# Optimization experiments

Measured on AMD Instinct MI355X. Metric: run time of the kernel, lower is better.

Reference implementation:

```python
import jax, jax.numpy as jnp
import numpy as np

SINKHORN_ITERS = 20
EPS = 1e-6


def setup_inputs() -> dict:
    key = jax.random.key(0)
    k1, k2 = jax.random.split(key)
    x = jax.random.normal(k1, (4, 4096, 4096), dtype=jnp.float32)
    W = jax.random.normal(k2, (4096, 4096), dtype=jnp.float32) * 0.02
    return {"x": x, "W": W}


def _sinkhorn(W):
    # W: [N, N] logits -> doubly-stochastic (Birkhoff) matrix, unit marginals
    P = jnp.exp(W)

    def body(_, P):
        P = P * (1.0 / (P.sum(axis=-2, keepdims=True) + EPS))  # column normalize
        P = P * (1.0 / (P.sum(axis=-1, keepdims=True) + EPS))  # row normalize
        return P

    return jax.lax.fori_loop(0, SINKHORN_ITERS, body, P)


def reference(x, W):
    W_proj = _sinkhorn(W)          # [N, N]
    out = jnp.matmul(x, W_proj)    # [B, S, N] @ [N, N] -> [B, S, N]
    return out
```

## Files before the change

kernel.cpp:

```cpp
#include <hip/hip_runtime.h>
#include <hip/hip_bf16.h>
#include <cstdint>
#include <cstddef>

#define NN 4096
#define SINK_ITERS 20
#define EPSV 1e-6f

typedef unsigned short u16;
typedef __attribute__((ext_vector_type(8))) short bf16x8;
typedef __attribute__((ext_vector_type(4))) short bf16x4;
typedef __attribute__((ext_vector_type(4))) float f32x4;

__device__ __forceinline__ float bf2f(u16 u) {
  union { unsigned int i; float f; } x; x.i = ((unsigned int)u) << 16; return x.f;
}
__device__ __forceinline__ u16 f2bf(float f) {
  union { float f; unsigned int i; } x; x.f = f;
  unsigned int i = x.i;
  unsigned int r = i + 0x7FFFu + ((i >> 16) & 1u);
  return (u16)(r >> 16);
}

typedef const __attribute__((address_space(1))) unsigned int* gas_p;
typedef __attribute__((address_space(3))) unsigned int* las_p;
__device__ __forceinline__ void gload16(const void* g, void* l) {
  __builtin_amdgcn_global_load_lds((gas_p)g, (las_p)l, 16, 0, 0);
}

__device__ __forceinline__ void gstore(float* p, float v) {
  __hip_atomic_store(p, v, __ATOMIC_RELAXED, __HIP_MEMORY_SCOPE_AGENT);
}
__device__ __forceinline__ float gloadc(const float* p) {
  return __hip_atomic_load(p, __ATOMIC_RELAXED, __HIP_MEMORY_SCOPE_AGENT);
}

#define SINK_WGS 256
#define SINK_SMEM (131072 + 1024 + 1024 + 8192)

__device__ __forceinline__ void gsyncF(unsigned* grp, int me, unsigned goal) {
  __syncthreads();
  int t = threadIdx.x;
  if (t < 64) {
    if (t == 0)
      __hip_atomic_store(grp + me, goal, __ATOMIC_RELAXED, __HIP_MEMORY_SCOPE_AGENT);
    unsigned v;
    long spin = 0;
    do {
      v = (t < 16) ? __hip_atomic_load(grp + t, __ATOMIC_RELAXED, __HIP_MEMORY_SCOPE_AGENT)
                   : goal;
    } while (__any(v < goal) && ++spin < 500000000L);
  }
  asm volatile("" ::: "memory");
  __syncthreads();
}

__global__ __launch_bounds__(512) void k_sinkhorn(
    const float* __restrict__ W, u16* __restrict__ Pt,
    float* __restrict__ Spart, float* __restrict__ Tpart, unsigned* bar) {
  extern __shared__ char smem[];
  u16* Kt = (u16*)smem;
  float* u_loc = (float*)(smem + 131072);
  float* v_loc = u_loc + 256;
  float* red = v_loc + 256;

  int wg = blockIdx.x;
  int a = wg >> 4, b = wg & 15;
  int i0 = a * 256, j0 = b * 256;
  int t = threadIdx.x;
  int lane = t & 63, wv = t >> 6;
  int cg = t & 31;

  unsigned* colbar = bar + b * 16;
  unsigned* rowbar = bar + (16 + a) * 16;

#pragma unroll
  for (int k = 0; k < 32; ++k) {
    int q = t + 512 * k;
    int il = q >> 6;
    int jc = (q & 63) << 2;
    f32x4 wvv = *(const f32x4*)(W + (size_t)(i0 + il) * NN + (j0 + jc));
    bf16x4 r;
#pragma unroll
    for (int c = 0; c < 4; ++c) r[c] = (short)f2bf(expf(wvv[c]));
    *(bf16x4*)(Kt + il * 256 + jc) = r;
  }
  if (t < 256) { u_loc[t] = 1.f; v_loc[t] = 1.f; }
  __syncthreads();

  for (int it = 0; it < SINK_ITERS; ++it) {
    int par = (it & 1) * 16;
    if (t < 256 && it > 0) {
      int pb = ((it - 1) & 1) * 16;
      float Ts = 0.f;
#pragma unroll
      for (int p = 0; p < 16; ++p) Ts += gloadc(&Tpart[(pb + p) * NN + i0 + t]);
      float ul = u_loc[t];
      u_loc[t] = ul / (ul * Ts + EPSV);
    }
    __syncthreads();

    float acc[8] = {0.f, 0.f, 0.f, 0.f, 0.f, 0.f, 0.f, 0.f};
#pragma unroll
    for (int k = 0; k < 16; ++k) {
      int row = (t >> 5) + 16 * k;
      bf16x8 kv = *(const bf16x8*)(Kt + row * 256 + cg * 8);
      float ui = u_loc[row];
#pragma unroll
      for (int c = 0; c < 8; ++c) acc[c] += ui * bf2f((u16)kv[c]);
    }
#pragma unroll
    for (int c = 0; c < 8; ++c) acc[c] += __shfl_xor(acc[c], 32, 64);
    if (lane < 32) {
#pragma unroll
      for (int c = 0; c < 8; ++c) red[wv * 256 + cg * 8 + c] = acc[c];
    }
    __syncthreads();
    if (t < 256) {
      float s = 0.f;
#pragma unroll
      for (int w = 0; w < 8; ++w) s += red[w * 256 + t];
      gstore(&Spart[(par + a) * NN + j0 + t], s);
    }
    gsyncF(colbar, a, (unsigned)(it + 1));

    if (t < 256) {
      float Ss = 0.f;
#pragma unroll
      for (int p = 0; p < 16; ++p) Ss += gloadc(&Spart[(par + p) * NN + j0 + t]);
      float vo = v_loc[t];
      v_loc[t] = vo / (vo * Ss + EPSV);
    }
    __syncthreads();

    f32x4 va = *(const f32x4*)(v_loc + cg * 8);
    f32x4 vb2 = *(const f32x4*)(v_loc + cg * 8 + 4);
    float tr[16];
#pragma unroll
    for (int k = 0; k < 16; ++k) {
      int row = (t >> 5) + 16 * k;
      bf16x8 kv = *(const bf16x8*)(Kt + row * 256 + cg * 8);
      float s = 0.f;
#pragma unroll
      for (int c = 0; c < 4; ++c) s += bf2f((u16)kv[c]) * va[c];
#pragma unroll
      for (int c = 0; c < 4; ++c) s += bf2f((u16)kv[4 + c]) * vb2[c];
      tr[k] = s;
    }
#pragma unroll
    for (int k = 0; k < 16; ++k) {
#pragma unroll
      for (int d = 1; d <= 16; d <<= 1) tr[k] += __shfl_xor(tr[k], d, 64);
    }
    if (lane == 0 || lane == 32) {
#pragma unroll
      for (int k = 0; k < 16; ++k) red[(t >> 5) + 16 * k] = tr[k];
    }
    __syncthreads();
    if (t < 256) gstore(&Tpart[(par + b) * NN + i0 + t], red[t]);
    gsyncF(rowbar, b, (unsigned)(it + 1));
  }

  if (t < 256) {
    int pb = ((SINK_ITERS - 1) & 1) * 16;
    float Ts = 0.f;
#pragma unroll
    for (int p = 0; p < 16; ++p) Ts += gloadc(&Tpart[(pb + p) * NN + i0 + t]);
    float ul = u_loc[t];
    u_loc[t] = ul / (ul * Ts + EPSV);
  }
  __syncthreads();

  {
    int jl = t & 255, h = t >> 8;
    float vv = v_loc[jl];
    size_t prow = (size_t)(j0 + jl) * NN + i0;
#pragma unroll
    for (int g = 0; g < 16; ++g) {
      int gg = h * 16 + g;
      int il0 = gg * 8;
      bf16x8 r;
#pragma unroll
      for (int e = 0; e < 8; ++e)
        r[e] = (short)f2bf(u_loc[il0 + e] * bf2f(Kt[(il0 + e) * 256 + jl]) * vv);
      *(bf16x8*)(Pt + prow + gg * 8) = r;
    }
  }
}

__global__ void k_f2bf(const float* __restrict__ X, u16* __restrict__ Xb, long n8) {
  long stride = (long)gridDim.x * blockDim.x;
  for (long i = (long)blockIdx.x * blockDim.x + threadIdx.x; i < n8; i += stride) {
    long idx = i * 8;
    f32x4 a = *(const f32x4*)(X + idx);
    f32x4 b = *(const f32x4*)(X + idx + 4);
    bf16x8 r;
#pragma unroll
    for (int c = 0; c < 4; ++c) r[c] = (short)f2bf(a[c]);
#pragma unroll
    for (int c = 0; c < 4; ++c) r[4 + c] = (short)f2bf(b[c]);
    *(bf16x8*)(Xb + idx) = r;
  }
}

#define GBM 256
#define GBN 256
#define GBK 64
#define GNT (NN / GBK)
#define GNT2 (GNT / 2)
#define GEMM_SMEM 131072

__global__ __launch_bounds__(512, 2) void k_gemm256(const u16* __restrict__ A,
                                                    const u16* __restrict__ Bt,
                                                    float* __restrict__ C) {
  extern __shared__ __align__(1024) char gsm[];

  int bid = blockIdx.x;
  int xcd = bid & 7, sidx = bid >> 3;
  int bm = (xcd << 3) | (sidx >> 4);
  int bn = sidx & 15;
  size_t m0 = (size_t)bm * GBM, n0 = (size_t)bn * GBN;

  int tid = threadIdx.x;
  int lane = tid & 63, w = tid >> 6;
  int wm = w >> 2, wn = w & 3;
  int l15 = lane & 15, kgb = (lane >> 4) * 16;
  int xk = kgb ^ (((l15 >> 3) & 1) << 5);

  int aoff[8], boff[4];
#pragma unroll
  for (int m = 0; m < 8; ++m) aoff[m] = (m * 16 + l15) * 64 + xk;
#pragma unroll
  for (int n = 0; n < 4; ++n) boff[n] = ((wn & 1) * 64 + n * 16 + l15) * 64 + xk;

  int dst2[2], sA[2][2], sB[2][2];
#pragma unroll
  for (int i = 0; i < 2; ++i) {
    int d = (i * 512 + tid) * 16;
    int L = d ^ (((d >> 9) & 1) << 5);
    int ks = L >> 13, r = (L >> 6) & 127, cb = L & 63;
    int kelem = ks * 32 + (cb >> 1);
    dst2[i] = d;
#pragma unroll
    for (int h = 0; h < 2; ++h) {
      sA[h][i] = (int)((m0 + h * 128 + r) * NN) + kelem;
      sB[h][i] = (int)((n0 + h * 128 + r) * NN) + kelem;
    }
  }

  f32x4 acc[8][4];
#pragma unroll
  for (int m = 0; m < 8; ++m)
#pragma unroll
    for (int n = 0; n < 4; ++n) acc[m][n] = (f32x4){0.f, 0.f, 0.f, 0.f};

#define ST_A(D, H, KT)                                                       \
  { char* b_ = gsm + (D) * 65536 + (H) * 16384;                              \
    gload16(A + (size_t)(sA[H][0] + (KT) * GBK), b_ + dst2[0]);              \
    gload16(A + (size_t)(sA[H][1] + (KT) * GBK), b_ + dst2[1]); }
#define ST_B(D, H, KT)                                                       \
  { char* b_ = gsm + (D) * 65536 + 32768 + (H) * 16384;                      \
    gload16(Bt + (size_t)(sB[H][0] + (KT) * GBK), b_ + dst2[0]);             \
    gload16(Bt + (size_t)(sB[H][1] + (KT) * GBK), b_ + dst2[1]); }

#define RD_A(BASE, M0)                                                       \
  _Pragma("unroll") for (int m = 0; m < 4; ++m)                              \
  _Pragma("unroll") for (int ks = 0; ks < 2; ++ks)                           \
      af[m][ks] = *(const bf16x8*)((BASE) + ks * 8192 + aoff[(M0) + m]);
#define RD_B(BASE, N0)                                                       \
  _Pragma("unroll") for (int n = 0; n < 2; ++n)                              \
  _Pragma("unroll") for (int ks = 0; ks < 2; ++ks)                           \
      bfr[(N0) + n][ks] = *(const bf16x8*)((BASE) + ks * 8192 + boff[(N0) + n]);
#define MM(AM, AN)                                                           \
  __builtin_amdgcn_s_setprio(1);                                             \
  _Pragma("unroll") for (int m = 0; m < 4; ++m)                              \
  _Pragma("unroll") for (int n = 0; n < 2; ++n)                              \
  _Pragma("unroll") for (int ks = 0; ks < 2; ++ks)                           \
      acc[(AM) + m][(AN) + n] = __builtin_amdgcn_mfma_f32_16x16x32_bf16(     \
          af[m][ks], bfr[(AN) + n][ks], acc[(AM) + m][(AN) + n], 0, 0, 0);   \
  __builtin_amdgcn_s_setprio(0);
#define BAR __builtin_amdgcn_s_barrier()
#define LGKM0 asm volatile("s_waitcnt lgkmcnt(0)" ::: "memory")

  ST_A(0, 0, 0) ST_A(0, 1, 0) ST_B(0, 0, 0) ST_B(0, 1, 0)
  ST_B(1, 0, 1) ST_B(1, 1, 1) ST_A(1, 0, 1)
  asm volatile("s_waitcnt vmcnt(6)" ::: "memory");
  BAR;

  for (int t2 = 0; t2 < GNT2; ++t2) {
    bool pf = (t2 < GNT2 - 1);
    int k1 = 2 * t2 + 1, k2 = 2 * t2 + 2, k3 = 2 * t2 + 3;

    {
      const char* Ab = gsm + wm * 16384;
      const char* Bb = gsm + 32768 + (wn >> 1) * 16384;
      bf16x8 af[4][2], bfr[4][2];

      RD_A(Ab, 0) RD_B(Bb, 0)
      ST_A(1, 1, k1)
      asm volatile("s_waitcnt lgkmcnt(8)" ::: "memory");
      BAR; LGKM0;
      MM(0, 0)
      BAR;

      RD_B(Bb, 2)
      BAR; LGKM0;
      MM(0, 2)
      BAR;

      RD_A(Ab, 4)
      if (pf) ST_B(0, 0, k2)
      BAR; LGKM0;
      MM(4, 2)
      BAR;

      if (pf) { ST_B(0, 1, k2) ST_A(0, 0, k2) }
      MM(4, 0)
      if (pf) { asm volatile("s_waitcnt vmcnt(6)" ::: "memory"); }
      else    { asm volatile("s_waitcnt vmcnt(0)" ::: "memory"); }
      BAR;
    }

    {
      const char* Ab = gsm + 65536 + wm * 16384;
      const char* Bb = gsm + 65536 + 32768 + (wn >> 1) * 16384;
      bf16x8 af[4][2], bfr[4][2];

      RD_A(Ab, 0) RD_B(Bb, 0)
      if (pf) ST_A(0, 1, k2)
      asm volatile("s_waitcnt lgkmcnt(8)" ::: "memory");
      BAR; LGKM0;
      MM(0, 0)
      BAR;

      RD_B(Bb, 2)
      BAR; LGKM0;
      MM(0, 2)
      BAR;

      RD_A(Ab, 4)
      if (pf) ST_B(1, 0, k3)
      BAR; LGKM0;
      MM(4, 2)
      BAR;

      if (pf) { ST_B(1, 1, k3) ST_A(1, 0, k3) }
      MM(4, 0)
      if (pf) { asm volatile("s_waitcnt vmcnt(6)" ::: "memory"); }
      else    { asm volatile("s_waitcnt vmcnt(0)" ::: "memory"); }
      BAR;
    }
  }
#undef ST_A
#undef ST_B
#undef RD_A
#undef RD_B
#undef MM
#undef BAR
#undef LGKM0

#pragma unroll
  for (int m = 0; m < 8; ++m) {
    size_t gr = m0 + (size_t)wm * 128 + m * 16 + (lane >> 4) * 4;
#pragma unroll
    for (int n = 0; n < 4; ++n) {
      size_t gc = n0 + (size_t)wn * 64 + n * 16 + l15;
#pragma unroll
      for (int i = 0; i < 4; ++i)
        C[(gr + i) * NN + gc] = acc[m][n][i];
    }
  }
}

#define BM 128
#define BN 128
#define BK 32
#define NT (NN / BK)

__global__ __launch_bounds__(256) void k_gemm(const u16* __restrict__ A,
                                              const u16* __restrict__ Bt,
                                              float* __restrict__ C) {
  __shared__ __align__(16) u16 lA[2][BM * BK];
  __shared__ __align__(16) u16 lB[2][BN * BK];

  int bid = blockIdx.x;
  int swz = (bid & 7) * 512 + (bid >> 3);
  int bm = swz >> 5, bn = swz & 31;

  int tid = threadIdx.x;
  int lane = tid & 63, w = tid >> 6;
  int wm = (w >> 1) * 64, wn = (w & 1) * 64;
  size_t m0 = (size_t)bm * BM, n0 = (size_t)bn * BN;

  f32x4 acc[4][4];
#pragma unroll
  for (int a = 0; a < 4; ++a)
#pragma unroll
    for (int b = 0; b < 4; ++b) acc[a][b] = (f32x4){0.f, 0.f, 0.f, 0.f};

  int srow = tid >> 2;
  int skc = (tid & 3) * 8;

  auto stage = [&](int buf, int t) {
    int k0 = t * BK;
#pragma unroll
    for (int it = 0; it < 2; ++it) {
      int row = it * 64 + srow;
      gload16(A + (m0 + row) * NN + k0 + skc, &lA[buf][row * BK + skc]);
      gload16(Bt + (n0 + row) * NN + k0 + skc, &lB[buf][row * BK + skc]);
    }
  };

  stage(0, 0);
  __syncthreads();

  int arow = wm + (lane & 15);
  int brow = wn + (lane & 15);
  int kc = (lane >> 4) * 8;

  for (int t = 0; t < NT; ++t) {
    int cur = t & 1;
    if (t < NT - 1) stage(cur ^ 1, t + 1);
    bf16x8 af[4], bfr[4];
#pragma unroll
    for (int f = 0; f < 4; ++f) {
      af[f] = *(const bf16x8*)&lA[cur][(arow + f * 16) * BK + kc];
      bfr[f] = *(const bf16x8*)&lB[cur][(brow + f * 16) * BK + kc];
    }
#pragma unroll
    for (int fm = 0; fm < 4; ++fm)
#pragma unroll
      for (int fn = 0; fn < 4; ++fn)
        acc[fm][fn] = __builtin_amdgcn_mfma_f32_16x16x32_bf16(af[fm], bfr[fn], acc[fm][fn], 0, 0, 0);
    __syncthreads();
  }

#pragma unroll
  for (int fm = 0; fm < 4; ++fm) {
    int r0 = wm + fm * 16 + (lane >> 4) * 4;
#pragma unroll
    for (int fn = 0; fn < 4; ++fn) {
      int c0 = wn + fn * 16 + (lane & 15);
#pragma unroll
      for (int i = 0; i < 4; ++i) {
        C[(m0 + r0 + i) * NN + n0 + c0] = acc[fm][fn][i];
      }
    }
  }
}

extern "C" void kernel_launch(void* const* d_in, const int* in_sizes, int n_in,
                              void* d_out, int out_size, void* d_ws, size_t ws_size,
                              hipStream_t stream) {
  const float* x = (const float*)d_in[0];
  const float* W = (const float*)d_in[1];
  float* out = (float*)d_out;

  char* ws = (char*)d_ws;
  const size_t XB_OFF = 0;
  const size_t PT_OFF = 134217728;
  const size_t SC_OFF = 167772160;
  if (ws_size < SC_OFF + (66 * (size_t)NN) * sizeof(float)) return;

  u16* xb = (u16*)(ws + XB_OFF);
  u16* Ptb = (u16*)(ws + PT_OFF);

  float* Sp = (float*)(ws + SC_OFF);
  float* Tp = Sp + 32 * NN;
  unsigned* bar = (unsigned*)(Tp + 32 * NN);

  k_f2bf<<<2048, 256, 0, stream>>>(x, xb, (long)out_size / 8);

  bool coop = true;
  int dev = 0;
  hipDeviceProp_t prop;
  if (hipGetDevice(&dev) != hipSuccess) coop = false;
  else if (hipGetDeviceProperties(&prop, dev) != hipSuccess) coop = false;
  else if (prop.multiProcessorCount < SINK_WGS) coop = false;
  if (coop && hipFuncSetAttribute((const void*)k_sinkhorn,
                                  hipFuncAttributeMaxDynamicSharedMemorySize,
                                  SINK_SMEM) != hipSuccess)
    coop = false;
  if (!coop) return;

  hipMemsetAsync(bar, 0, 32 * 16 * sizeof(unsigned), stream);
  k_sinkhorn<<<SINK_WGS, 512, SINK_SMEM, stream>>>(W, Ptb, Sp, Tp, bar);

  bool big = (hipFuncSetAttribute((const void*)k_gemm256,
                                  hipFuncAttributeMaxDynamicSharedMemorySize,
                                  GEMM_SMEM) == hipSuccess);
  if (big) {
    k_gemm256<<<1024, 512, GEMM_SMEM, stream>>>(xb, Ptb, out);
    if (hipGetLastError() != hipSuccess) big = false;
  }
  if (!big) k_gemm<<<4096, 256, 0, stream>>>(xb, Ptb, out);
}
```

Baseline: 708.7 us.

## Software-pipeline LDS fragment reads across MFMA phases in GEMM main loop

Restructures the double-buffered GEMM main loop so LDS fragment reads for the next MFMA phase are issued before the current phase's MFMAs, using separate register sets per phase. Global prefetch of a whole k-tile is now issued in one group, and the next buffer's first fragments are loaded before the last MFMA group. This is meant to hide LDS latency behind matrix math and cut barrier stalls. It costs more VGPRs, which may lower occupancy or cause spills.

```diff
diff --git a/kernel.cpp b/kernel.cpp
--- a/kernel.cpp
+++ b/kernel.cpp
@@ -248,11 +248,18 @@
     }
   }
 
+  const char* Ab0 = gsm + wm * 16384;
+  const char* Bb0 = gsm + 32768 + (wn >> 1) * 16384;
+  const char* Ab1 = gsm + 65536 + wm * 16384;
+  const char* Bb1 = gsm + 65536 + 32768 + (wn >> 1) * 16384;
+
   f32x4 acc[8][4];
 #pragma unroll
   for (int m = 0; m < 8; ++m)
 #pragma unroll
     for (int n = 0; n < 4; ++n) acc[m][n] = (f32x4){0.f, 0.f, 0.f, 0.f};
+
+  bf16x8 af0[4][2], af4[4][2], bA0[2][2], bA1[2][2], bB[2][2];
 
 #define ST_A(D, H, KT)                                                       \
   { char* b_ = gsm + (D) * 65536 + (H) * 16384;                              \
@@ -262,102 +269,84 @@
   { char* b_ = gsm + (D) * 65536 + 32768 + (H) * 16384;                      \
     gload16(Bt + (size_t)(sB[H][0] + (KT) * GBK), b_ + dst2[0]);             \
     gload16(Bt + (size_t)(sB[H][1] + (KT) * GBK), b_ + dst2[1]); }
-
-#define RD_A(BASE, M0)                                                       \
+#define ST8(D, KT) ST_A(D, 0, KT) ST_A(D, 1, KT) ST_B(D, 0, KT) ST_B(D, 1, KT)
+
+#define RD_A(BASE, M0, DEST)                                                 \
   _Pragma("unroll") for (int m = 0; m < 4; ++m)                              \
   _Pragma("unroll") for (int ks = 0; ks < 2; ++ks)                           \
-      af[m][ks] = *(const bf16x8*)((BASE) + ks * 8192 + aoff[(M0) + m]);
-#define RD_B(BASE, N0)                                                       \
+      DEST[m][ks] = *(const bf16x8*)((BASE) + ks * 8192 + aoff[(M0) + m]);
+#define RD_B2(BASE, N0, DEST)                                                \
   _Pragma("unroll") for (int n = 0; n < 2; ++n)                              \
   _Pragma("unroll") for (int ks = 0; ks < 2; ++ks)                           \
-      bfr[(N0) + n][ks] = *(const bf16x8*)((BASE) + ks * 8192 + boff[(N0) + n]);
-#define MM(AM, AN)                                                           \
+      DEST[n][ks] = *(const bf16x8*)((BASE) + ks * 8192 + boff[(N0) + n]);
+#define MM(AF, BV, AM, AN)                                                   \
   __builtin_amdgcn_s_setprio(1);                                             \
   _Pragma("unroll") for (int m = 0; m < 4; ++m)                              \
   _Pragma("unroll") for (int n = 0; n < 2; ++n)                              \
   _Pragma("unroll") for (int ks = 0; ks < 2; ++ks)                           \
       acc[(AM) + m][(AN) + n] = __builtin_amdgcn_mfma_f32_16x16x32_bf16(     \
-          af[m][ks], bfr[(AN) + n][ks], acc[(AM) + m][(AN) + n], 0, 0, 0);   \
+          AF[m][ks], BV[n][ks], acc[(AM) + m][(AN) + n], 0, 0, 0);           \
   __builtin_amdgcn_s_setprio(0);
 #define BAR __builtin_amdgcn_s_barrier()
 #define LGKM0 asm volatile("s_waitcnt lgkmcnt(0)" ::: "memory")
-
-  ST_A(0, 0, 0) ST_A(0, 1, 0) ST_B(0, 0, 0) ST_B(0, 1, 0)
-  ST_B(1, 0, 1) ST_B(1, 1, 1) ST_A(1, 0, 1)
-  asm volatile("s_waitcnt vmcnt(6)" ::: "memory");
+#define VM8 asm volatile("s_waitcnt vmcnt(8)" ::: "memory")
+#define VM0 asm volatile("s_waitcnt vmcnt(0)" ::: "memory")
+
+  ST8(0, 0) ST8(1, 1)
+  VM8;
   BAR;
+  RD_A(Ab0, 0, af0) RD_B2(Bb0, 0, bA0)
 
   for (int t2 = 0; t2 < GNT2; ++t2) {
     bool pf = (t2 < GNT2 - 1);
-    int k1 = 2 * t2 + 1, k2 = 2 * t2 + 2, k3 = 2 * t2 + 3;
-
-    {
-      const char* Ab = gsm + wm * 16384;
-      const char* Bb = gsm + 32768 + (wn >> 1) * 16384;
-      bf16x8 af[4][2], bfr[4][2];
-
-      RD_A(Ab, 0) RD_B(Bb, 0)
-      ST_A(1, 1, k1)
-      asm volatile("s_waitcnt lgkmcnt(8)" ::: "memory");
-      BAR; LGKM0;
-      MM(0, 0)
-      BAR;
-
-      RD_B(Bb, 2)
-      BAR; LGKM0;
-      MM(0, 2)
-      BAR;
-
-      RD_A(Ab, 4)
-      if (pf) ST_B(0, 0, k2)
-      BAR; LGKM0;
-      MM(4, 2)
-      BAR;
-
-      if (pf) { ST_B(0, 1, k2) ST_A(0, 0, k2) }
-      MM(4, 0)
-      if (pf) { asm volatile("s_waitcnt vmcnt(6)" ::: "memory"); }
-      else    { asm volatile("s_waitcnt vmcnt(0)" ::: "memory"); }
-      BAR;
-    }
-
-    {
-      const char* Ab = gsm + 65536 + wm * 16384;
-      const char* Bb = gsm + 65536 + 32768 + (wn >> 1) * 16384;
-      bf16x8 af[4][2], bfr[4][2];
-
-      RD_A(Ab, 0) RD_B(Bb, 0)
-      if (pf) ST_A(0, 1, k2)
-      asm volatile("s_waitcnt lgkmcnt(8)" ::: "memory");
-      BAR; LGKM0;
-      MM(0, 0)
-      BAR;
-
-      RD_B(Bb, 2)
-      BAR; LGKM0;
-      MM(0, 2)
-      BAR;
-
-      RD_A(Ab, 4)
-      if (pf) ST_B(1, 0, k3)
-      BAR; LGKM0;
-      MM(4, 2)
-      BAR;
-
-      if (pf) { ST_B(1, 1, k3) ST_A(1, 0, k3) }
-      MM(4, 0)
-      if (pf) { asm volatile("s_waitcnt vmcnt(6)" ::: "memory"); }
-      else    { asm volatile("s_waitcnt vmcnt(0)" ::: "memory"); }
-      BAR;
-    }
+    int k2 = 2 * t2 + 2, k3 = 2 * t2 + 3;
+
+    LGKM0;
+    RD_B2(Bb0, 2, bB)
+    MM(af0, bA0, 0, 0)
+    BAR;
+    LGKM0;
+    RD_A(Ab0, 4, af4)
+    MM(af0, bB, 0, 2)
+    BAR;
+    LGKM0;
+    if (pf) ST8(0, k2)
+    MM(af4, bB, 4, 2)
+    BAR;
+    if (pf) { VM8; } else { VM0; }
+    BAR;
+    RD_A(Ab1, 0, af0) RD_B2(Bb1, 0, bA1)
+    MM(af4, bA0, 4, 0)
+    BAR;
+
+    LGKM0;
+    RD_B2(Bb1, 2, bB)
+    MM(af0, bA1, 0, 0)
+    BAR;
+    LGKM0;
+    RD_A(Ab1, 4, af4)
+    MM(af0, bB, 0, 2)
+    BAR;
+    LGKM0;
+    if (pf) ST8(1, k3)
+    MM(af4, bB, 4, 2)
+    BAR;
+    if (pf) { VM8; } else { VM0; }
+    BAR;
+    if (pf) { RD_A(Ab0, 0, af0) RD_B2(Bb0, 0, bA0) }
+    MM(af4, bA1, 4, 0)
+    BAR;
   }
 #undef ST_A
 #undef ST_B
+#undef ST8
 #undef RD_A
-#undef RD_B
+#undef RD_B2
 #undef MM
 #undef BAR
 #undef LGKM0
+#undef VM8
+#undef VM0
 
 #pragma unroll
   for (int m = 0; m < 8; ++m) {
```

New measurement: 814.2 us. 1.15x slower.
